# Kernel optimization log

Hardware: AMD Instinct MI355X
Metric: run time of the kernel (lower is better)

## Reference

```python
import jax, jax.numpy as jnp
import numpy as np
import math

K, D_FEAT, L_FAC, N = 128, 1024, 16, 16384


def setup_inputs() -> dict:
    key = jax.random.key(0)
    k1, k2, k3, k4 = jax.random.split(key, 4)
    x = jax.random.normal(k1, (N, D_FEAT), dtype=jnp.float32)
    MU = 0.1 * jax.random.normal(k2, (K, D_FEAT), dtype=jnp.float32)
    A = 0.05 * jax.random.normal(k3, (K, D_FEAT, L_FAC), dtype=jnp.float32)
    # D must be positive (it is a per-feature noise std): uniform in [0.1, 0.5]
    D = jax.random.uniform(k4, (K, D_FEAT), dtype=jnp.float32, minval=0.1, maxval=0.5)
    PI = jnp.ones((K,), dtype=jnp.float32) / K
    return {"x": x, "PI": PI, "MU": MU, "A": A, "D": D}


def reference(x, PI, MU, A, D):
    # Faithful vectorized version of MFA._per_component_log_likelihood.
    k, d, l = A.shape
    iD = jnp.power(D, -2.0)                      # (K, d)  = 1/D^2
    iDA = iD[:, :, None] * A                     # (K, d, l)
    # Woodbury small matrix: L = I_l + A^T (iD * A)
    Lm = jnp.eye(l, dtype=A.dtype)[None] + jnp.einsum('kdl,kdm->klm', A, iDA)
    iL = jnp.linalg.inv(Lm)                      # (K, l, l)

    # y[k,n,:] = A^T (iD * (x_n - MU_k))  without materializing (K,N,d)
    y = jnp.einsum('nd,kdl->knl', x, iDA) - jnp.einsum('kd,kdl->kl', MU, iDA)[:, None, :]
    # term1[k,n] = sum_d iD[k,d] * (x_n - MU_k)^2, expanded to avoid (K,N,d)
    term1 = (jnp.einsum('nd,kd->kn', x * x, iD)
             - 2.0 * jnp.einsum('nd,kd->kn', x, iD * MU)
             + jnp.sum(iD * MU * MU, axis=1)[:, None])
    # quadratic correction: y^T iL y
    quad = jnp.einsum('knl,klm,knm->kn', y, iL, y)
    m_d = term1 - quad                           # (K, N) Mahalanobis distances

    det_L = jnp.linalg.slogdet(Lm)[1]            # (K,)
    log_det_Sigma = det_L - jnp.sum(jnp.log(iD), axis=1)
    log2pi = jnp.asarray(math.log(2.0 * math.pi), dtype=x.dtype)
    log_prob = -0.5 * ((d * log2pi + log_det_Sigma)[:, None] + m_d)  # (K, N)
    # NOTE: original adds raw PI (not log PI) -- replicated faithfully.
    return PI[None, :] + log_prob.T              # (N, K)
```

## Files before the change

### kernel.cpp

```cpp
#include <hip/hip_runtime.h>
#include <math.h>

typedef unsigned short ushort_t;
typedef unsigned char  uchar_t;
typedef __attribute__((ext_vector_type(8))) short short8v;
typedef __attribute__((ext_vector_type(4))) float f32x4;
typedef __attribute__((ext_vector_type(2))) long l64x2;

#define KCOMP 128
#define DF    1024
#define LF    16
#define NPTS  16384
#define LOG2PI 1.8378770664093453f

#define XQ_OFF    ((size_t)0)
#define XQ_BYTES  ((size_t)NPTS*DF)
#define BQ_OFF    (XQ_OFF + XQ_BYTES)
#define BQ_BYTES  ((size_t)2048*DF)
#define BSK_OFF   (BQ_OFF + BQ_BYTES)
#define BSK_BYTES ((size_t)KCOMP*2*DF*2)
#define CSK_OFF   (BSK_OFF + BSK_BYTES)
#define FULL_NEED (CSK_OFF + 512)

__device__ __forceinline__ ushort_t f2bf(float f) {
  union { float f; unsigned u; } v; v.f = f;
  unsigned u = v.u;
  return (ushort_t)((u + 0x7FFFu + ((u >> 16) & 1u)) >> 16);
}

#define GLOAD16(gp, lp) __builtin_amdgcn_global_load_lds( \
  (const __attribute__((address_space(1))) unsigned int*)(gp), \
  (__attribute__((address_space(3))) unsigned int*)(lp), 16, 0, 0)

#define DPPADD(x, ctrl) do { \
  int _yi = __builtin_amdgcn_update_dpp(0, __float_as_int(x), ctrl, 0xF, 0xF, true); \
  (x) += __int_as_float(_yi); } while (0)

__global__ __launch_bounds__(256) void mfa_pre(
    const float* __restrict__ PI, const float* __restrict__ MU,
    const float* __restrict__ A, const float* __restrict__ Dm,
    uchar_t* __restrict__ Bq, ushort_t* __restrict__ Bsk,
    float* __restrict__ csk)
{
  const int k = blockIdx.x, t = threadIdx.x;
  const int tl = t >> 4, tm = t & 15;
  __shared__ float As[64][16];
  __shared__ float iD64[64], MU64[64];
  __shared__ float R[16][17];
  __shared__ float rinv_s[16], zsh[16], bsh[16];
  __shared__ float red[64];
  __shared__ float sc_sumlog, sc_c3;

  float accL = 0.f, accb = 0.f, c3p = 0.f, slogp = 0.f;
  for (int ch = 0; ch < 16; ++ch) {
    __syncthreads();
    ((float4*)&As[0][0])[t] =
        ((const float4*)(A + (size_t)k*DF*LF + (size_t)ch*1024))[t];
    if (t < 64) {
      float dv = Dm[k*DF + ch*64 + t];
      iD64[t] = 1.f/(dv*dv);
      MU64[t] = MU[k*DF + ch*64 + t];
    }
    __syncthreads();
    #pragma unroll 4
    for (int dd = 0; dd < 64; ++dd)
      accL = fmaf(As[dd][tl]*iD64[dd], As[dd][tm], accL);
    if (tm == 0)
      for (int dd = 0; dd < 64; ++dd)
        accb = fmaf(iD64[dd]*MU64[dd], As[dd][tl], accb);
    if (t < 64) {
      c3p = fmaf(iD64[t]*MU64[t], MU64[t], c3p);
      slogp += logf(iD64[t]);
    }
  }
  __syncthreads();
  R[tl][tm] = accL + (tl == tm ? 1.f : 0.f);
  if (tm == 0) bsh[tl] = accb;
  if (t < 64) red[t] = slogp;
  __syncthreads();
  if (t == 0) { float s = 0.f; for (int i = 0; i < 64; ++i) s += red[i]; sc_sumlog = s; }
  __syncthreads();
  if (t < 64) red[t] = c3p;
  __syncthreads();
  if (t == 0) { float s = 0.f; for (int i = 0; i < 64; ++i) s += red[i]; sc_c3 = s; }

  for (int j = 0; j < 16; ++j) {
    __syncthreads();
    if (t == j) {
      float s = R[j][j];
      for (int i = 0; i < j; ++i) s -= R[j][i]*R[j][i];
      float rj = sqrtf(s);
      R[j][j] = rj; rinv_s[j] = 1.f/rj;
    }
    __syncthreads();
    if (t < 16 && t > j) {
      float s = R[t][j];
      for (int i = 0; i < j; ++i) s -= R[t][i]*R[j][i];
      R[t][j] = s * rinv_s[j];
    }
  }
  __syncthreads();
  if (t == 0) {
    float ldet = 0.f;
    for (int j = 0; j < 16; ++j) ldet += 2.f*logf(R[j][j]);
    float w[16], z[16];
    for (int j = 0; j < 16; ++j) {
      float s = bsh[j];
      for (int i = 0; i < j; ++i) s -= R[j][i]*w[i];
      w[j] = s*rinv_s[j];
    }
    for (int j = 15; j >= 0; --j) {
      float s = w[j];
      for (int i = j+1; i < 16; ++i) s -= R[i][j]*z[i];
      z[j] = s*rinv_s[j];
      zsh[j] = z[j];
    }
    float muh = sc_c3;
    for (int l = 0; l < 16; ++l) muh -= bsh[l]*zsh[l];
    csk[k] = PI[k] - 0.5f*((float)DF*LOG2PI + ldet - sc_sumlog) - 0.5f*muh;
  }
  __syncthreads();

  for (int it = 0; it < 4; ++it) {
    const int d = t + it*256;
    float dv = Dm[k*DF + d];
    float iD = 1.f/(dv*dv);
    float mu = MU[k*DF + d];
    float v[16], gg[16];
    #pragma unroll
    for (int l = 0; l < 16; ++l) v[l] = iD * A[((size_t)k*DF + d)*LF + l];
    #pragma unroll
    for (int j = 0; j < 16; ++j) {
      float s = v[j];
      #pragma unroll
      for (int i = 0; i < 16; ++i) if (i < j) s -= R[j][i]*gg[i];
      gg[j] = s * rinv_s[j];
    }
    float h = iD*mu;
    #pragma unroll
    for (int l = 0; l < 16; ++l) h -= v[l]*zsh[l];
    const int dd = d & 63;
    const size_t poff = (size_t)(d & ~63) + ((dd >> 3) & 3)*16 + (dd >> 5)*8 + (dd & 7);
    #pragma unroll
    for (int l = 0; l < 16; ++l) {
      int r8 = __builtin_amdgcn_cvt_pk_fp8_f32(gg[l], gg[l], 0, false);
      Bq[(size_t)(k*16 + l)*DF + poff] = (uchar_t)(r8 & 0xFF);
    }
    Bsk[(size_t)k*2*DF + d]      = f2bf(-2.f*h);
    Bsk[(size_t)k*2*DF + DF + d] = f2bf(iD);
  }
}

__global__ __launch_bounds__(512) void mfa_sk5(
    const float* __restrict__ x, const ushort_t* __restrict__ Bsk,
    const float* __restrict__ csk, uchar_t* __restrict__ xq,
    float* __restrict__ out)
{
  __shared__ ushort_t xs[4096];
  __shared__ ushort_t x2s[4096];
  __shared__ ushort_t Bs[16384];
  const int t = threadIdx.x, lane = t & 63, wid = t >> 6;
  const int wc = wid & 3, rgrp = wid >> 2;
  const int lr = lane & 15, lh = lane >> 4;
  const int n0 = blockIdx.x * 64;
  const int xr = t >> 3, c8 = t & 7;

  f32x4 acc[2][2] = {};

  float4 v0, v1;
  {
    const float* xp = x + (size_t)(n0 + xr)*DF + c8*8;
    v0 = ((const float4*)xp)[0]; v1 = ((const float4*)xp)[1];
  }

  for (int tt = 0; tt < 16; ++tt) {
    const int d0 = tt * 64;
    __syncthreads();
    long xq_pack;
    {
      float e[8] = {v0.x,v0.y,v0.z,v0.w, v1.x,v1.y,v1.z,v1.w};
      short8v b, q;
      #pragma unroll
      for (int i = 0; i < 8; ++i) {
        b[i] = (short)f2bf(e[i]);
        q[i] = (short)f2bf(e[i]*e[i]);
      }
      const int ch = c8 ^ (xr & 7);
      *(short8v*)&xs[xr*64 + ch*8]  = b;
      *(short8v*)&x2s[xr*64 + ch*8] = q;
      int p0 = 0, p1 = 0;
      p0 = __builtin_amdgcn_cvt_pk_fp8_f32(e[0], e[1], p0, false);
      p0 = __builtin_amdgcn_cvt_pk_fp8_f32(e[2], e[3], p0, true);
      p1 = __builtin_amdgcn_cvt_pk_fp8_f32(e[4], e[5], p1, false);
      p1 = __builtin_amdgcn_cvt_pk_fp8_f32(e[6], e[7], p1, true);
      xq_pack = (long)(((unsigned long long)(unsigned)p1 << 32) | (unsigned)p0);
    }
    #pragma unroll
    for (int jj = 0; jj < 4; ++jj) {
      int id = wid*4 + jj;
      int vc = id*8 + (lane >> 3);
      int g = (lane & 7) ^ (vc & 7);
      const ushort_t* src = (vc < 128)
        ? Bsk + (size_t)vc*(2*DF) + d0 + g*8
        : Bsk + (size_t)(vc - 128)*(2*DF) + DF + d0 + g*8;
      GLOAD16(src, (char*)Bs + id*1024);
    }
    asm volatile("s_waitcnt vmcnt(0) lgkmcnt(0)" ::: "memory");
    __syncthreads();
    {
      const size_t perm = (size_t)(c8 & 3)*16 + (size_t)(c8 >> 2)*8;
      *(long*)&xq[(size_t)(n0 + xr)*DF + d0 + perm] = xq_pack;
    }
    if (tt < 15) {
      const float* xp = x + (size_t)(n0 + xr)*DF + (d0 + 64) + c8*8;
      v0 = ((const float4*)xp)[0]; v1 = ((const float4*)xp)[1];
    }
    __builtin_amdgcn_sched_barrier(0);
    #pragma unroll
    for (int ks = 0; ks < 2; ++ks) {
      const int cterm = ((ks*4 + lh) ^ (lr & 7)) * 8;
      short8v a_[2], a2_[2], bh[2], bi[2];
      #pragma unroll
      for (int rb = 0; rb < 2; ++rb) {
        int row = rgrp*32 + rb*16 + lr;
        a_[rb]  = *(const short8v*)&xs[row*64 + cterm];
        a2_[rb] = *(const short8v*)&x2s[row*64 + cterm];
      }
      #pragma unroll
      for (int cb = 0; cb < 2; ++cb) {
        int vh = wc*32 + cb*16 + lr;
        bh[cb] = *(const short8v*)&Bs[vh*64 + cterm];
        bi[cb] = *(const short8v*)&Bs[(128 + vh)*64 + cterm];
      }
      #pragma unroll
      for (int cb = 0; cb < 2; ++cb)
        #pragma unroll
        for (int rb = 0; rb < 2; ++rb) {
          acc[rb][cb] = __builtin_amdgcn_mfma_f32_16x16x32_bf16(a_[rb],  bh[cb], acc[rb][cb], 0,0,0);
          acc[rb][cb] = __builtin_amdgcn_mfma_f32_16x16x32_bf16(a2_[rb], bi[cb], acc[rb][cb], 0,0,0);
        }
    }
  }
  #pragma unroll
  for (int cb = 0; cb < 2; ++cb) {
    int comp = wc*32 + cb*16 + lr;
    float ck = csk[comp];
    #pragma unroll
    for (int rb = 0; rb < 2; ++rb)
      #pragma unroll
      for (int j = 0; j < 4; ++j) {
        int row = n0 + rgrp*32 + rb*16 + lh*4 + j;
        out[(size_t)row*KCOMP + comp] = ck - 0.5f*acc[rb][cb][j];
      }
  }
}

__global__ __launch_bounds__(512, 4) void mfa_gemm11(
    const uchar_t* __restrict__ xq, const uchar_t* __restrict__ Bq,
    float* __restrict__ out)
{
  __shared__ uchar_t smem[73728];
  const int t = threadIdx.x, lane = t & 63, wid = t >> 6;
  const int wm = wid & 1, wn = wid >> 1;
  const int lr = lane & 15, lh = lane >> 4;

  const int bid = blockIdx.x;
  const int xcd = bid & 7, ib = bid >> 3;
  const int rb = xcd*16 + (ib >> 3);
  const int cb = ib & 7;
  const int n0 = rb * 128, c0 = cb * 256;

  f32x4 acc[4][4] = {};

  const int js = (((lane & 3) ^ ((lane >> 3) & 3)) * 16);
  const uchar_t* srcP[3]; int dstO[3];
  #pragma unroll
  for (int q = 0; q < 3; ++q) {
    int id = wid*3 + q;
    if (id < 8) {
      int r = id*16 + (lane >> 2);
      srcP[q] = xq + (size_t)(n0 + r)*DF + js;
      dstO[q] = id*1024;
    } else {
      int cr = (id - 8)*16 + (lane >> 2);
      srcP[q] = Bq + (size_t)(c0 + cr)*DF + js;
      dstO[q] = 8192 + (id - 8)*1024;
    }
  }
  const int rsw = (lh ^ ((lr >> 1) & 3)) * 16;
  const int aO = (wm*64 + lr)*64 + rsw;
  const int bO = 8192 + (wn*64 + lr)*64 + rsw;

  #define STAGE11(slot, tt_) do { \
    _Pragma("unroll") \
    for (int q = 0; q < 3; ++q) \
      GLOAD16(srcP[q] + (tt_)*64, (char*)smem + (slot)*24576 + dstO[q] + ((lane)*16 & 1023)); \
  } while (0)

  STAGE11(0, 0);
  STAGE11(1, 1);

  for (int tt = 0; tt < 16; ++tt) {
    if (tt < 15) asm volatile("s_waitcnt vmcnt(3)" ::: "memory");
    else         asm volatile("s_waitcnt vmcnt(0)" ::: "memory");
    __builtin_amdgcn_s_barrier();
    if (tt + 2 <= 15) STAGE11((tt + 2) % 3, tt + 2);

    const char* lb = (const char*)smem + (tt % 3) * 24576;
    l64x2 a2[4], b2[4];
    #pragma unroll
    for (int rt = 0; rt < 4; ++rt) a2[rt] = *(const l64x2*)(lb + aO + rt*1024);
    #pragma unroll
    for (int ct = 0; ct < 4; ++ct) b2[ct] = *(const l64x2*)(lb + bO + ct*1024);

    __builtin_amdgcn_s_setprio(1);
    #pragma unroll
    for (int ct = 0; ct < 4; ++ct)
      #pragma unroll
      for (int rt = 0; rt < 4; ++rt)
        acc[rt][ct] = __builtin_amdgcn_mfma_f32_16x16x32_fp8_fp8(a2[rt][0], b2[ct][0], acc[rt][ct], 0,0,0);
    #pragma unroll
    for (int ct = 0; ct < 4; ++ct)
      #pragma unroll
      for (int rt = 0; rt < 4; ++rt)
        acc[rt][ct] = __builtin_amdgcn_mfma_f32_16x16x32_fp8_fp8(a2[rt][1], b2[ct][1], acc[rt][ct], 0,0,0);
    __builtin_amdgcn_s_setprio(0);
  }

  #pragma unroll
  for (int ct = 0; ct < 4; ++ct) {
    const int comp = cb*16 + wn*4 + ct;
    #pragma unroll
    for (int rt = 0; rt < 4; ++rt) {
      #pragma unroll
      for (int j = 0; j < 4; ++j) {
        float v = acc[rt][ct][j];
        float sq = v*v;
        DPPADD(sq, 0xB1);
        DPPADD(sq, 0x4E);
        DPPADD(sq, 0x124);
        DPPADD(sq, 0x128);
        if (lr == 0) {
          int row = n0 + wm*64 + rt*16 + lh*4 + j;
          size_t idx = (size_t)row * KCOMP + comp;
          out[idx] = out[idx] + 0.5f*sq;
        }
      }
    }
  }
}

#define FB_NG 8
#define FB_CG 288
#define FB_BN 128
#define FB_DT 32
#define FB_PITCH 40
#define FB_BMAT_ELEMS ((size_t)(FB_NG*FB_CG)*DF)
#define FB_CST_OFF (FB_BMAT_ELEMS*2)
#define FB_MUH_OFF (FB_CST_OFF + 512)

__global__ __launch_bounds__(256) void fb_pre(
    const float* __restrict__ PI, const float* __restrict__ MU,
    const float* __restrict__ A, const float* __restrict__ Dm,
    ushort_t* __restrict__ Bmat, float* __restrict__ cst, float* __restrict__ muh)
{
  const int k = blockIdx.x, t = threadIdx.x;
  const int tl = t >> 4, tm = t & 15;
  __shared__ float As[16][16], iDsh[16], MUsh[16];
  __shared__ float R[16][17], rinv[16], zsh[16], bsh[16];
  __shared__ float red[256];

  float accL = 0.f, accb = 0.f, slog = 0.f;
  for (int d0 = 0; d0 < DF; d0 += 16) {
    __syncthreads();
    As[tl][tm] = A[((size_t)k*DF + d0 + tl)*LF + tm];
    if (t < 16) {
      float dv = Dm[k*DF + d0 + t];
      iDsh[t] = 1.f/(dv*dv);
      MUsh[t] = MU[k*DF + d0 + t];
    }
    __syncthreads();
    #pragma unroll
    for (int dd = 0; dd < 16; ++dd)
      accL = fmaf(As[dd][tl]*iDsh[dd], As[dd][tm], accL);
    if (tm == 0) {
      #pragma unroll
      for (int dd = 0; dd < 16; ++dd)
        accb = fmaf(iDsh[dd]*MUsh[dd], As[dd][tl], accb);
    }
    if (t < 16) slog += logf(iDsh[t]);
  }
  __syncthreads();
  R[tl][tm] = accL + (tl == tm ? 1.f : 0.f);
  if (tm == 0) bsh[tl] = accb;
  red[t] = (t < 16) ? slog : 0.f;
  __syncthreads();
  float sumlogiD = 0.f;
  if (t == 0) { for (int i = 0; i < 16; ++i) sumlogiD += red[i]; }

  for (int j = 0; j < 16; ++j) {
    if (t == j) {
      float s = R[j][j];
      for (int i = 0; i < j; ++i) s -= R[j][i]*R[j][i];
      float rj = sqrtf(s);
      R[j][j] = rj; rinv[j] = 1.f/rj;
    }
    __syncthreads();
    if (t < 16 && t > j) {
      float s = R[t][j];
      for (int i = 0; i < j; ++i) s -= R[t][i]*R[j][i];
      R[t][j] = s * rinv[j];
    }
    __syncthreads();
  }

  float ldet = 0.f;
  if (t == 0) {
    #pragma unroll
    for (int j = 0; j < 16; ++j) ldet += 2.f*logf(R[j][j]);
    float w[16], z[16];
    #pragma unroll
    for (int j = 0; j < 16; ++j) {
      float s = bsh[j];
      #pragma unroll
      for (int i = 0; i < 16; ++i) if (i < j) s -= R[j][i]*w[i];
      w[j] = s*rinv[j];
    }
    #pragma unroll
    for (int j = 15; j >= 0; --j) {
      float s = w[j];
      #pragma unroll
      for (int i = 0; i < 16; ++i) if (i > j) s -= R[i][j]*z[i];
      z[j] = s*rinv[j];
      zsh[j] = z[j];
    }
  }
  __syncthreads();

  const int g = k >> 4, kl = k & 15;
  ushort_t* Bgp = Bmat + (size_t)g*FB_CG*DF;
  float muhp = 0.f;
  for (int itr = 0; itr < 4; ++itr) {
    int d = t + itr*256;
    float dv = Dm[k*DF + d];
    float iD = 1.f/(dv*dv);
    float mu = MU[k*DF + d];
    float v[16], gg[16];
    #pragma unroll
    for (int l = 0; l < 16; ++l) v[l] = iD * A[((size_t)k*DF + d)*LF + l];
    #pragma unroll
    for (int j = 0; j < 16; ++j) {
      float s = v[j];
      #pragma unroll
      for (int i = 0; i < 16; ++i) if (i < j) s -= R[j][i]*gg[i];
      gg[j] = s * rinv[j];
    }
    float h = iD*mu;
    #pragma unroll
    for (int l = 0; l < 16; ++l) h -= v[l]*zsh[l];
    muhp = fmaf(mu, h, muhp);
    #pragma unroll
    for (int l = 0; l < 16; ++l)
      Bgp[(size_t)(kl*16 + l)*DF + d] = f2bf(gg[l]);
    Bgp[(size_t)(256 + kl)*DF + d] = f2bf(h);
    Bgp[(size_t)(272 + kl)*DF + d] = f2bf(iD);
  }
  red[t] = muhp;
  __syncthreads();
  for (int s = 128; s > 0; s >>= 1) {
    if (t < s) red[t] += red[t + s];
    __syncthreads();
  }
  if (t == 0) {
    muh[k] = red[0];
    cst[k] = PI[k] - 0.5f*((float)DF*LOG2PI + ldet - sumlogiD);
  }
}

__global__ __launch_bounds__(512, 2) void fb_main(
    const float* __restrict__ x, const ushort_t* __restrict__ Bmat,
    const float* __restrict__ cst, const float* __restrict__ muh,
    float* __restrict__ out)
{
  __shared__ __align__(16) ushort_t smem[2*FB_BN*FB_PITCH + FB_CG*FB_PITCH];
  ushort_t* xs  = smem;
  ushort_t* x2s = smem + FB_BN*FB_PITCH;
  ushort_t* Bs  = smem + 2*FB_BN*FB_PITCH;

  const int t = threadIdx.x;
  const int lane = t & 63, wid = t >> 6;
  const int wr = wid & 3, wc = wid >> 2;
  const int lr = lane & 15, lh = lane >> 4;
  const int n0 = blockIdx.x * FB_BN;
  const int g  = blockIdx.y;

  f32x4 acc[2][9] = {};
  const int srow = t >> 2, sc = t & 3;

  int xoff[2];
  #pragma unroll
  for (int rt = 0; rt < 2; ++rt)
    xoff[rt] = (wr*32 + rt*16 + lr)*FB_PITCH + lh*8;
  int boff[9];
  #pragma unroll
  for (int ct = 0; ct < 9; ++ct)
    boff[ct] = (wc*144 + ct*16 + lr)*FB_PITCH + lh*8;

  for (int d0 = 0; d0 < DF; d0 += FB_DT) {
    __syncthreads();
    {
      const float* xp = x + (size_t)(n0 + srow)*DF + d0 + sc*8;
      float4 v0 = *(const float4*)xp;
      float4 v1 = *(const float4*)(xp + 4);
      float e[8] = {v0.x,v0.y,v0.z,v0.w,v1.x,v1.y,v1.z,v1.w};
      short8v xv, qv;
      #pragma unroll
      for (int i = 0; i < 8; ++i) {
        xv[i] = (short)f2bf(e[i]);
        qv[i] = (short)f2bf(e[i]*e[i]);
      }
      *(short8v*)&xs[srow*FB_PITCH + sc*8]  = xv;
      *(short8v*)&x2s[srow*FB_PITCH + sc*8] = qv;
    }
    for (int u = t; u < FB_CG*4; u += 512) {
      int col = u >> 2, c = u & 3;
      *(short8v*)&Bs[col*FB_PITCH + c*8] =
        *(const short8v*)&Bmat[((size_t)(g*FB_CG + col))*DF + d0 + c*8];
    }
    __syncthreads();

    short8v xf[2];
    #pragma unroll
    for (int rt = 0; rt < 2; ++rt) xf[rt] = *(short8v*)&xs[xoff[rt]];
    #pragma unroll
    for (int ct = 0; ct < 8; ++ct) {
      short8v bfr = *(short8v*)&Bs[boff[ct]];
      #pragma unroll
      for (int rt = 0; rt < 2; ++rt)
        acc[rt][ct] = __builtin_amdgcn_mfma_f32_16x16x32_bf16(xf[rt], bfr, acc[rt][ct], 0, 0, 0);
    }
    {
      short8v bfr = *(short8v*)&Bs[boff[8]];
      short8v a0 = xf[0], a1 = xf[1];
      if (wc) {
        a0 = *(short8v*)&x2s[xoff[0]];
        a1 = *(short8v*)&x2s[xoff[1]];
      }
      acc[0][8] = __builtin_amdgcn_mfma_f32_16x16x32_bf16(a0, bfr, acc[0][8], 0, 0, 0);
      acc[1][8] = __builtin_amdgcn_mfma_f32_16x16x32_bf16(a1, bfr, acc[1][8], 0, 0, 0);
    }
  }

  __syncthreads();
  float* s1v = (float*)smem;
  float* s2h = s1v + FB_BN*17;
  if (wc == 1) {
    #pragma unroll
    for (int rt = 0; rt < 2; ++rt)
      #pragma unroll
      for (int j = 0; j < 4; ++j) {
        int row = wr*32 + rt*16 + lh*4 + j;
        s2h[row*17 + lr] = acc[rt][7][j];
        s1v[row*17 + lr] = acc[rt][8][j];
      }
  }
  __syncthreads();

  const int nyt = wc ? 7 : 9;
  #pragma unroll
  for (int ct = 0; ct < 9; ++ct) {
    if (ct < nyt) {
      int comp = wc*9 + ct;
      int kk = g*16 + comp;
      float cstk = cst[kk], muhk = muh[kk];
      #pragma unroll
      for (int rt = 0; rt < 2; ++rt)
        #pragma unroll
        for (int j = 0; j < 4; ++j) {
          float yv = acc[rt][ct][j];
          float sq = yv*yv;
          sq += __shfl_xor(sq, 1);
          sq += __shfl_xor(sq, 2);
          sq += __shfl_xor(sq, 4);
          sq += __shfl_xor(sq, 8);
          int row = wr*32 + rt*16 + lh*4 + j;
          float s1 = s1v[row*17 + comp];
          float s2 = s2h[row*17 + comp];
          float res = cstk - 0.5f*(s1 - sq - 2.f*s2 + muhk);
          if (lr == 0) out[(size_t)(n0 + row)*KCOMP + kk] = res;
        }
    }
  }
}

extern "C" void kernel_launch(void* const* d_in, const int* in_sizes, int n_in,
                              void* d_out, int out_size, void* d_ws, size_t ws_size,
                              hipStream_t stream) {
  const float* x  = (const float*)d_in[0];
  const float* PI = (const float*)d_in[1];
  const float* MU = (const float*)d_in[2];
  const float* A  = (const float*)d_in[3];
  const float* Dm = (const float*)d_in[4];
  float* out = (float*)d_out;

  if (ws_size >= FULL_NEED) {
    uchar_t* xq   = (uchar_t*)((char*)d_ws + XQ_OFF);
    uchar_t* Bq   = (uchar_t*)((char*)d_ws + BQ_OFF);
    ushort_t* Bsk = (ushort_t*)((char*)d_ws + BSK_OFF);
    float* csk    = (float*)((char*)d_ws + CSK_OFF);

    mfa_pre<<<dim3(KCOMP), dim3(256), 0, stream>>>(PI, MU, A, Dm, Bq, Bsk, csk);
    mfa_sk5<<<dim3(NPTS/64), dim3(512), 0, stream>>>(x, Bsk, csk, xq, out);
    mfa_gemm11<<<dim3((NPTS/128)*(2048/256)), dim3(512), 0, stream>>>(xq, Bq, out);
  } else {
    ushort_t* Bmat = (ushort_t*)d_ws;
    float* cstp = (float*)((char*)d_ws + FB_CST_OFF);
    float* muhp = (float*)((char*)d_ws + FB_MUH_OFF);
    fb_pre<<<dim3(KCOMP), dim3(256), 0, stream>>>(PI, MU, A, Dm, Bmat, cstp, muhp);
    fb_main<<<dim3(NPTS/FB_BN, FB_NG), dim3(512), 0, stream>>>(x, Bmat, cstp, muhp, out);
  }
}
```

Measured before the change: 149.0 us.

## Widen mfa_pre to 1024 threads and stage whole A slice in LDS

The per-component preprocessing kernel now runs 1024 threads per block instead of 256. It loads the full A, iD and MU slices into shared memory at once instead of streaming 16 chunks, and splits the d-reduction of the Woodbury matrix across four thread groups. The final per-d loop runs once per thread and reads iD and MU from shared memory. The aim is to shorten the serial prologue kernel, which runs only 128 blocks, at the cost of about 72KB of LDS per block and extra reduction barriers.

Result: faster. 129.5 us (-13.1%).

```diff
diff --git a/kernel.cpp b/kernel.cpp
--- a/kernel.cpp
+++ b/kernel.cpp
@@ -36,53 +36,77 @@
   int _yi = __builtin_amdgcn_update_dpp(0, __float_as_int(x), ctrl, 0xF, 0xF, true); \
   (x) += __int_as_float(_yi); } while (0)
 
-__global__ __launch_bounds__(256) void mfa_pre(
+__global__ __launch_bounds__(1024) void mfa_pre(
     const float* __restrict__ PI, const float* __restrict__ MU,
     const float* __restrict__ A, const float* __restrict__ Dm,
     uchar_t* __restrict__ Bq, ushort_t* __restrict__ Bsk,
     float* __restrict__ csk)
 {
   const int k = blockIdx.x, t = threadIdx.x;
-  const int tl = t >> 4, tm = t & 15;
-  __shared__ float As[64][16];
-  __shared__ float iD64[64], MU64[64];
+  __shared__ float As[DF*LF];
+  __shared__ float iDs[DF];
+  __shared__ float MUs[DF];
+  __shared__ float red[1024];
+  __shared__ float bpart[4][16];
   __shared__ float R[16][17];
   __shared__ float rinv_s[16], zsh[16], bsh[16];
-  __shared__ float red[64];
   __shared__ float sc_sumlog, sc_c3;
 
-  float accL = 0.f, accb = 0.f, c3p = 0.f, slogp = 0.f;
-  for (int ch = 0; ch < 16; ++ch) {
-    __syncthreads();
-    ((float4*)&As[0][0])[t] =
-        ((const float4*)(A + (size_t)k*DF*LF + (size_t)ch*1024))[t];
-    if (t < 64) {
-      float dv = Dm[k*DF + ch*64 + t];
-      iD64[t] = 1.f/(dv*dv);
-      MU64[t] = MU[k*DF + ch*64 + t];
-    }
-    __syncthreads();
+  {
+    const float4* Ag = (const float4*)(A + (size_t)k*DF*LF);
+    float4* Al = (float4*)As;
+    #pragma unroll
+    for (int i = 0; i < 4; ++i) Al[t + i*1024] = Ag[t + i*1024];
+    float dv = Dm[(size_t)k*DF + t];
+    iDs[t] = 1.f/(dv*dv);
+    MUs[t] = MU[(size_t)k*DF + t];
+  }
+  __syncthreads();
+
+  const int e = t & 255, q = t >> 8;
+  const int tl = e >> 4, tm = e & 15;
+  {
+    float acc = 0.f;
+    const int d0 = q*256;
     #pragma unroll 4
-    for (int dd = 0; dd < 64; ++dd)
-      accL = fmaf(As[dd][tl]*iD64[dd], As[dd][tm], accL);
-    if (tm == 0)
-      for (int dd = 0; dd < 64; ++dd)
-        accb = fmaf(iD64[dd]*MU64[dd], As[dd][tl], accb);
-    if (t < 64) {
-      c3p = fmaf(iD64[t]*MU64[t], MU64[t], c3p);
-      slogp += logf(iD64[t]);
-    }
-  }
-  __syncthreads();
-  R[tl][tm] = accL + (tl == tm ? 1.f : 0.f);
-  if (tm == 0) bsh[tl] = accb;
-  if (t < 64) red[t] = slogp;
+    for (int dd = 0; dd < 256; ++dd) {
+      int d = d0 + dd;
+      acc = fmaf(As[d*16+tl]*iDs[d], As[d*16+tm], acc);
+    }
+    red[t] = acc;
+  }
+  if (e < 16) {
+    float accb = 0.f;
+    const int d0 = q*256;
+    for (int dd = 0; dd < 256; ++dd) {
+      int d = d0 + dd;
+      accb = fmaf(iDs[d]*MUs[d], As[d*16+e], accb);
+    }
+    bpart[q][e] = accb;
+  }
+  __syncthreads();
+  if (q == 0) {
+    float s = red[e] + red[e+256] + red[e+512] + red[e+768];
+    R[tl][tm] = s + (tl == tm ? 1.f : 0.f);
+  }
+  if (t < 16) bsh[t] = bpart[0][t] + bpart[1][t] + bpart[2][t] + bpart[3][t];
+  __syncthreads();
+
+  red[t] = iDs[t]*MUs[t]*MUs[t];
+  __syncthreads();
+  if (t < 256) red[t] = red[t] + red[t+256] + red[t+512] + red[t+768];
+  __syncthreads();
+  if (t < 64) red[t] = red[t] + red[t+64] + red[t+128] + red[t+192];
+  __syncthreads();
+  if (t == 0) { float s = 0.f; for (int i = 0; i < 64; ++i) s += red[i]; sc_c3 = s; }
+  __syncthreads();
+  red[t] = logf(iDs[t]);
+  __syncthreads();
+  if (t < 256) red[t] = red[t] + red[t+256] + red[t+512] + red[t+768];
+  __syncthreads();
+  if (t < 64) red[t] = red[t] + red[t+64] + red[t+128] + red[t+192];
   __syncthreads();
   if (t == 0) { float s = 0.f; for (int i = 0; i < 64; ++i) s += red[i]; sc_sumlog = s; }
-  __syncthreads();
-  if (t < 64) red[t] = c3p;
-  __syncthreads();
-  if (t == 0) { float s = 0.f; for (int i = 0; i < 64; ++i) s += red[i]; sc_c3 = s; }
 
   for (int j = 0; j < 16; ++j) {
     __syncthreads();
@@ -121,11 +145,10 @@
   }
   __syncthreads();
 
-  for (int it = 0; it < 4; ++it) {
-    const int d = t + it*256;
-    float dv = Dm[k*DF + d];
-    float iD = 1.f/(dv*dv);
-    float mu = MU[k*DF + d];
+  {
+    const int d = t;
+    float iD = iDs[d];
+    float mu = MUs[d];
     float v[16], gg[16];
     #pragma unroll
     for (int l = 0; l < 16; ++l) v[l] = iD * A[((size_t)k*DF + d)*LF + l];
@@ -609,7 +632,7 @@
     ushort_t* Bsk = (ushort_t*)((char*)d_ws + BSK_OFF);
     float* csk    = (float*)((char*)d_ws + CSK_OFF);
 
-    mfa_pre<<<dim3(KCOMP), dim3(256), 0, stream>>>(PI, MU, A, Dm, Bq, Bsk, csk);
+    mfa_pre<<<dim3(KCOMP), dim3(1024), 0, stream>>>(PI, MU, A, Dm, Bq, Bsk, csk);
     mfa_sk5<<<dim3(NPTS/64), dim3(512), 0, stream>>>(x, Bsk, csk, xq, out);
     mfa_gemm11<<<dim3((NPTS/128)*(2048/256)), dim3(512), 0, stream>>>(xq, Bq, out);
   } else {
```
